# Kernel optimization log

Hardware: AMD Instinct MI355X
Metric: run time of the kernel (lower is better)

## Reference

```python
import jax, jax.numpy as jnp
import numpy as np

N = 10000
E = 160000
C = 256        # in_channels
M = 256        # mid_channels
R = 64         # nregion


def _glorot(key, shape):
    fan_in, fan_out = shape[-1], shape[0]
    lim = (6.0 / (fan_in + fan_out)) ** 0.5
    return jax.random.uniform(key, shape, jnp.float32, -lim, lim)


def setup_inputs() -> dict:
    key = jax.random.key(0)
    ks = jax.random.split(key, 12)
    x = jax.random.normal(ks[0], (N, C), jnp.float32)
    edge_index = jax.random.randint(ks[1], (2, E), 0, N, jnp.int32)
    conv_w = _glorot(ks[2], (C, C))
    conv_b = jnp.zeros((C,), jnp.float32)
    lin1_w = _glorot(ks[3], (M, C)); lin1_b = jnp.zeros((M,), jnp.float32)
    lin2_w = _glorot(ks[4], (M, M)); lin2_b = jnp.zeros((M,), jnp.float32)
    lin3_w = _glorot(ks[5], (1, M)); lin3_b = jnp.zeros((1,), jnp.float32)
    lin4_w = _glorot(ks[6], (M, M)); lin4_b = jnp.zeros((M,), jnp.float32)
    bilin_w = _glorot(ks[7], (R, M, M)) * 0.1
    bilin_b = jnp.zeros((R,), jnp.float32)
    return {"x": x, "edge_index": edge_index,
            "conv_w": conv_w, "conv_b": conv_b,
            "lin1_w": lin1_w, "lin1_b": lin1_b,
            "lin2_w": lin2_w, "lin2_b": lin2_b,
            "lin3_w": lin3_w, "lin3_b": lin3_b,
            "lin4_w": lin4_w, "lin4_b": lin4_b,
            "bilin_w": bilin_w, "bilin_b": bilin_b}


def gcn_conv(x, edge_index, w, b):
    # PyG GCNConv: add self-loops, symmetric D^-1/2 (A+I) D^-1/2 normalization
    src, dst = edge_index[0], edge_index[1]
    n = x.shape[0]
    xw = x @ w.T                                            # [N, C]
    deg = jnp.ones((n,), xw.dtype).at[dst].add(jnp.ones((E,), xw.dtype))  # +1 for self loop
    dinv = jax.lax.rsqrt(deg)
    norm = dinv[src] * dinv[dst]                            # [E]
    agg = jnp.zeros_like(xw).at[dst].add(norm[:, None] * xw[src])
    agg = agg + (dinv * dinv)[:, None] * xw                 # self-loop messages
    return agg + b


def reference(x, edge_index, conv_w, conv_b, lin1_w, lin1_b, lin2_w, lin2_b,
              lin3_w, lin3_b, lin4_w, lin4_b, bilin_w, bilin_b):
    out = jax.nn.relu(gcn_conv(x, edge_index, conv_w, conv_b))
    x0 = out + x                                            # residual [N, C]
    x0 = jax.nn.relu(x0 @ lin1_w.T + lin1_b)                # [N, M]
    x1 = jax.nn.relu(x0 @ lin2_w.T + lin2_b)
    x1 = x1 @ lin3_w.T + lin3_b                             # [N, 1]
    x2 = jax.nn.relu(x0 @ lin4_w.T + lin4_b)                # [N, M]
    # Bilinear(x2, x2): out[n,r] = x2[n] @ W[r] @ x2[n] + b[r]
    t = (x2 @ bilin_w.reshape(R * M, M).T).reshape(-1, R, M)  # [N, R, M]
    x2 = jnp.sum(t * x2[:, None, :], axis=-1) + bilin_b       # [N, R]
    return (x1, x2)
```

## Files before the change

kernel.cpp:

```cpp
#include <hip/hip_runtime.h>

typedef unsigned short u16;
typedef __attribute__((ext_vector_type(8))) short bf16x8;
typedef __attribute__((ext_vector_type(4))) float f32x4;

#define N_NODES 10000
#define E_EDGES 160000

__device__ __forceinline__ float b2f(u16 u) {
  union { unsigned i; float f; } c; c.i = ((unsigned)u) << 16; return c.f;
}
__device__ __forceinline__ u16 f2b(float f) {
  union { float f; unsigned i; } c; c.f = f;
  unsigned i = c.i;
  return (u16)((i + 0x7FFFu + ((i >> 16) & 1u)) >> 16);
}

__global__ void detect_kernel(const unsigned* __restrict__ w, int* __restrict__ flag) {
  int t = threadIdx.x;
  int cnt = 0;
  for (int i = t; i < 1024; i += 64) {
    unsigned e = (w[i] >> 7) & 0xFF;
    cnt += (e >= 100 && e <= 145) ? 1 : 0;
  }
  for (int o = 32; o; o >>= 1) cnt += __shfl_xor(cnt, o);
  if (t == 0) *flag = (cnt >= 512) ? 1 : 0;
}
__global__ void canon_kernel(const void* __restrict__ src, u16* __restrict__ dst,
                             int n, const int* __restrict__ flag) {
  int i = blockIdx.x * 256 + threadIdx.x;
  if (i >= n) return;
  if (*flag) dst[i] = ((const u16*)src)[i];
  else       dst[i] = f2b(((const float*)src)[i]);
}
__global__ void canon4_kernel(const void* s0, const void* s1, const void* s2, const void* s3,
                              u16* d0, u16* d1, u16* d2, u16* d3,
                              const int* __restrict__ flag) {
  int tsel = blockIdx.x >> 8;
  int i = (blockIdx.x & 255) * 256 + threadIdx.x;
  const void* s = tsel == 0 ? s0 : tsel == 1 ? s1 : tsel == 2 ? s2 : s3;
  u16* d = tsel == 0 ? d0 : tsel == 1 ? d1 : tsel == 2 ? d2 : d3;
  if (*flag) d[i] = ((const u16*)s)[i];
  else       d[i] = f2b(((const float*)s)[i]);
}
__global__ void canon_small_kernel(const void* s0, const void* s1, const void* s2,
                                   const void* s3, const void* s4, const void* s5,
                                   const void* s6,
                                   u16* d0, u16* d1, u16* d2, u16* d3, u16* d4,
                                   u16* d5, u16* d6, const int* __restrict__ flag) {
  int t = threadIdx.x;
  int f = *flag;
  const void* srcs[7] = {s0, s1, s2, s3, s4, s5, s6};
  u16* dsts[7] = {d0, d1, d2, d3, d4, d5, d6};
  const int ns[7] = {256, 256, 256, 256, 256, 64, 1};
#pragma unroll
  for (int k = 0; k < 7; ++k) {
    if (t < ns[k]) {
      if (f) dsts[k][t] = ((const u16*)srcs[k])[t];
      else   dsts[k][t] = f2b(((const float*)srcs[k])[t]);
    }
  }
}

__device__ __forceinline__ void stage_async(const u16* __restrict__ src, int stride,
                                            int row0, int maxRow, int k0,
                                            u16* lds, int w, int lane) {
  int rsel = lane >> 3;
  int gch = (lane & 7) ^ rsel;
#pragma unroll
  for (int i = 0; i < 4; ++i) {
    int rb = (w * 4 + i) * 8;
    int grow = row0 + rb + rsel;
    grow = grow > maxRow ? maxRow : grow;
    const u16* gp = src + (size_t)grow * stride + k0 + gch * 8;
    u16* lp = lds + rb * 64;
    __builtin_amdgcn_global_load_lds(
        (const __attribute__((address_space(1))) void*)gp,
        (__attribute__((address_space(3))) void*)lp, 16, 0, 0);
  }
}

__device__ __forceinline__ void mma_tile(const u16* lA, const u16* lB,
                                         f32x4 acc[4][4], int wr, int wc, int lane) {
#pragma unroll
  for (int ks = 0; ks < 2; ++ks) {
    bf16x8 af[4], bfr[4];
    int g = ks * 4 + (lane >> 4);
#pragma unroll
    for (int t = 0; t < 4; ++t) {
      int rowA = wr * 64 + t * 16 + (lane & 15);
      af[t] = *(const bf16x8*)(lA + rowA * 64 + ((g ^ (rowA & 7)) * 8));
      int rowB = wc * 64 + t * 16 + (lane & 15);
      bfr[t] = *(const bf16x8*)(lB + rowB * 64 + ((g ^ (rowB & 7)) * 8));
    }
#pragma unroll
    for (int ti = 0; ti < 4; ++ti)
#pragma unroll
      for (int tj = 0; tj < 4; ++tj)
        acc[ti][tj] = __builtin_amdgcn_mfma_f32_16x16x32_bf16(af[ti], bfr[tj],
                                                              acc[ti][tj], 0, 0, 0);
  }
}

template <bool RELU, bool F32OUT>
__global__ __launch_bounds__(256, 2)
void gemm_kernel(const u16* __restrict__ A, const u16* __restrict__ B,
                 const u16* __restrict__ bias, float* __restrict__ outF,
                 u16* __restrict__ outB, int NN, int J, int K) {
  __shared__ u16 lA[128 * 64];
  __shared__ u16 lB[128 * 64];
  int lane = threadIdx.x & 63;
  int w = threadIdx.x >> 6;
  int wr = w >> 1, wc = w & 1;
  int n0 = blockIdx.y * 128;
  int j0 = blockIdx.x * 128;
  f32x4 acc[4][4];
#pragma unroll
  for (int i = 0; i < 4; ++i)
#pragma unroll
    for (int j = 0; j < 4; ++j) acc[i][j] = (f32x4){0.f, 0.f, 0.f, 0.f};

  for (int kt = 0; kt < K; kt += 64) {
    stage_async(A, K, n0, NN - 1, kt, lA, w, lane);
    stage_async(B, K, j0, J - 1, kt, lB, w, lane);
    __syncthreads();
    mma_tile(lA, lB, acc, wr, wc, lane);
    __syncthreads();
  }

#pragma unroll
  for (int ti = 0; ti < 4; ++ti)
#pragma unroll
    for (int tj = 0; tj < 4; ++tj) {
      int col = j0 + wc * 64 + tj * 16 + (lane & 15);
      float bv = bias ? b2f(bias[col]) : 0.0f;
#pragma unroll
      for (int r = 0; r < 4; ++r) {
        int row = n0 + wr * 64 + ti * 16 + ((lane >> 4) << 2) + r;
        if (row < NN) {
          float v = acc[ti][tj][r] + bv;
          if (RELU) v = fmaxf(v, 0.0f);
          if (F32OUT) outF[(size_t)row * J + col] = v;
          else        outB[(size_t)row * J + col] = f2b(v);
        }
      }
    }
}

__global__ __launch_bounds__(256, 2)
void gemm_fused234_kernel(const u16* __restrict__ A, const u16* __restrict__ B,
                          const u16* __restrict__ bias, const u16* __restrict__ w3,
                          float* __restrict__ out1acc, u16* __restrict__ x2v, int NN) {
  __shared__ u16 lA[128 * 64];
  __shared__ u16 lB[128 * 64];
  int lane = threadIdx.x & 63;
  int w = threadIdx.x >> 6;
  int wr = w >> 1, wc = w & 1;
  int n0 = blockIdx.y * 128;
  int j0 = blockIdx.x * 128;
  f32x4 acc[4][4];
#pragma unroll
  for (int i = 0; i < 4; ++i)
#pragma unroll
    for (int j = 0; j < 4; ++j) acc[i][j] = (f32x4){0.f, 0.f, 0.f, 0.f};

  for (int kt = 0; kt < 256; kt += 64) {
    stage_async(A, 256, n0, NN - 1, kt, lA, w, lane);
    stage_async(B, 256, j0, 511, kt, lB, w, lane);
    __syncthreads();
    mma_tile(lA, lB, acc, wr, wc, lane);
    __syncthreads();
  }

  if (j0 < 256) {
    float part[4][4];
#pragma unroll
    for (int ti = 0; ti < 4; ++ti)
#pragma unroll
      for (int r = 0; r < 4; ++r) part[ti][r] = 0.0f;
#pragma unroll
    for (int ti = 0; ti < 4; ++ti)
#pragma unroll
      for (int tj = 0; tj < 4; ++tj) {
        int col = j0 + wc * 64 + tj * 16 + (lane & 15);
        float bv = b2f(bias[col]);
        float wv = b2f(w3[col]);
#pragma unroll
        for (int r = 0; r < 4; ++r) {
          float v = fmaxf(acc[ti][tj][r] + bv, 0.0f);
          part[ti][r] += v * wv;
        }
      }
#pragma unroll
    for (int ti = 0; ti < 4; ++ti)
#pragma unroll
      for (int r = 0; r < 4; ++r) {
        float s = part[ti][r];
        s += __shfl_xor(s, 1);
        s += __shfl_xor(s, 2);
        s += __shfl_xor(s, 4);
        s += __shfl_xor(s, 8);
        if ((lane & 15) == 0) {
          int row = n0 + wr * 64 + ti * 16 + ((lane >> 4) << 2) + r;
          if (row < NN) unsafeAtomicAdd(&out1acc[row], s);
        }
      }
  } else {
#pragma unroll
    for (int ti = 0; ti < 4; ++ti)
#pragma unroll
      for (int tj = 0; tj < 4; ++tj) {
        int col = j0 + wc * 64 + tj * 16 + (lane & 15);
        float bv = b2f(bias[col]);
#pragma unroll
        for (int r = 0; r < 4; ++r) {
          int row = n0 + wr * 64 + ti * 16 + ((lane >> 4) << 2) + r;
          if (row < NN) {
            float v = fmaxf(acc[ti][tj][r] + bv, 0.0f);
            x2v[(size_t)row * 256 + (col - 256)] = f2b(v);
          }
        }
      }
  }
}

__global__ __launch_bounds__(256, 2)
void bilinear_kernel(const u16* __restrict__ x2v, const u16* __restrict__ W,
                     float* __restrict__ out2acc, int NN) {
  __shared__ u16 lA[128 * 64];
  __shared__ u16 lB[128 * 64];
  int lane = threadIdx.x & 63;
  int w = threadIdx.x >> 6;
  int wr = w >> 1, wc = w & 1;
  int n0 = blockIdx.y * 128;
  int rm0 = blockIdx.x * 128;
  int m0g = rm0 & 255;
  int xv_kt = (m0g >> 6) + wc;
  f32x4 acc[4][4];
#pragma unroll
  for (int i = 0; i < 4; ++i)
#pragma unroll
    for (int j = 0; j < 4; ++j) acc[i][j] = (f32x4){0.f, 0.f, 0.f, 0.f};

  u16 xvr[4][16];

#pragma unroll
  for (int kt4 = 0; kt4 < 4; ++kt4) {
    stage_async(x2v, 256, n0, NN - 1, kt4 * 64, lA, w, lane);
    stage_async(W, 256, rm0, 16383, kt4 * 64, lB, w, lane);
    __syncthreads();
    mma_tile(lA, lB, acc, wr, wc, lane);
    if (kt4 == xv_kt) {
#pragma unroll
      for (int tj = 0; tj < 4; ++tj) {
        int kl = tj * 16 + (lane & 15);
        int ch = kl >> 3, off = kl & 7;
#pragma unroll
        for (int ti = 0; ti < 4; ++ti)
#pragma unroll
          for (int r = 0; r < 4; ++r) {
            int rowl = wr * 64 + ti * 16 + ((lane >> 4) << 2) + r;
            xvr[tj][ti * 4 + r] = lA[rowl * 64 + ((ch ^ (rowl & 7)) * 8) + off];
          }
      }
    }
    __syncthreads();
  }

  int region = rm0 >> 8;
  float rowsum[4][4];
#pragma unroll
  for (int ti = 0; ti < 4; ++ti)
#pragma unroll
    for (int r = 0; r < 4; ++r) rowsum[ti][r] = 0.0f;

#pragma unroll
  for (int ti = 0; ti < 4; ++ti)
#pragma unroll
    for (int tj = 0; tj < 4; ++tj)
#pragma unroll
      for (int r = 0; r < 4; ++r)
        rowsum[ti][r] += acc[ti][tj][r] * b2f(xvr[tj][ti * 4 + r]);

#pragma unroll
  for (int ti = 0; ti < 4; ++ti)
#pragma unroll
    for (int r = 0; r < 4; ++r) {
      float s = rowsum[ti][r];
      s += __shfl_xor(s, 1);
      s += __shfl_xor(s, 2);
      s += __shfl_xor(s, 4);
      s += __shfl_xor(s, 8);
      if ((lane & 15) == 0) {
        int rowl = wr * 64 + ti * 16 + ((lane >> 4) << 2) + r;
        int n = n0 + rowl;
        if (n < NN) unsafeAtomicAdd(&out2acc[(size_t)n * 64 + region], s);
      }
    }
}

__global__ void hist_kernel(const int* __restrict__ ei, int* __restrict__ count) {
  int i = blockIdx.x * 256 + threadIdx.x;
  if (i < E_EDGES) atomicAdd(&count[ei[E_EDGES + i]], 1);
}

__global__ void scan_kernel(const int* __restrict__ count, int* __restrict__ start,
                            int* __restrict__ cursor, float* __restrict__ dinv) {
  __shared__ int wsum[16];
  __shared__ int carry_s;
  int t = threadIdx.x;
  int wv = t >> 6, ln = t & 63;
  if (t == 0) carry_s = 0;
  __syncthreads();
  for (int base = 0; base < N_NODES; base += 1024) {
    int i = base + t;
    int v = (i < N_NODES) ? count[i] : 0;
    int s = v;
#pragma unroll
    for (int o = 1; o < 64; o <<= 1) {
      int u = __shfl_up(s, o);
      if (ln >= o) s += u;
    }
    if (ln == 63) wsum[wv] = s;
    __syncthreads();
    if (wv == 0) {
      int x = (ln < 16) ? wsum[ln] : 0;
#pragma unroll
      for (int o = 1; o < 16; o <<= 1) {
        int u = __shfl_up(x, o);
        if (ln >= o) x += u;
      }
      if (ln < 16) wsum[ln] = x;
    }
    __syncthreads();
    int excl = s - v + (wv ? wsum[wv - 1] : 0) + carry_s;
    if (i < N_NODES) {
      start[i] = excl;
      cursor[i] = excl;
      dinv[i] = rsqrtf(1.0f + (float)v);
    }
    __syncthreads();
    if (t == 0) carry_s += wsum[15];
    __syncthreads();
  }
}

__global__ void place_kernel(const int* __restrict__ ei, int* __restrict__ cursor,
                             int* __restrict__ order) {
  int i = blockIdx.x * 256 + threadIdx.x;
  if (i >= E_EDGES) return;
  int d = ei[E_EDGES + i];
  int pos = atomicAdd(&cursor[d], 1);
  order[pos] = i;
}

__global__ void gather_kernel(const int* __restrict__ ei, const int* __restrict__ order,
                              const int* __restrict__ start, const int* __restrict__ count,
                              const float* __restrict__ dinv, const float* __restrict__ xw,
                              const u16* __restrict__ conv_b, const u16* __restrict__ x,
                              u16* __restrict__ x0) {
  int node = (blockIdx.x * blockDim.x + threadIdx.x) >> 6;
  int lane = threadIdx.x & 63;
  if (node >= N_NODES) return;
  int s0 = start[node], cnt = count[node];
  float dn = dinv[node];
  float ax = 0.f, ay = 0.f, az = 0.f, aw = 0.f;
  for (int base = 0; base < cnt; base += 64) {
    int rem = cnt - base;
    int m = rem < 64 ? rem : 64;
    int eid = (lane < m) ? order[s0 + base + lane] : 0;
    int s = (lane < m) ? ei[eid] : 0;
    float nrm = (lane < m) ? dinv[s] * dn : 0.f;
    for (int j = 0; j < m; ++j) {
      int sj = __shfl(s, j);
      float nj = __shfl(nrm, j);
      float4 v = *((const float4*)(xw + (size_t)sj * 256) + lane);
      ax += nj * v.x; ay += nj * v.y; az += nj * v.z; aw += nj * v.w;
    }
  }
  float4 sv = *((const float4*)(xw + (size_t)node * 256) + lane);
  float slw = dn * dn;
  const u16* bb = conv_b + lane * 4;
  const u16* xr = x + (size_t)node * 256 + lane * 4;
  u16 o[4];
  float vals[4] = {ax + slw * sv.x, ay + slw * sv.y, az + slw * sv.z, aw + slw * sv.w};
#pragma unroll
  for (int j = 0; j < 4; ++j) {
    float v = vals[j] + b2f(bb[j]);
    v = fmaxf(v, 0.0f) + b2f(xr[j]);
    o[j] = f2b(v);
  }
  *((ushort4*)(x0 + (size_t)node * 256) + lane) = make_ushort4(o[0], o[1], o[2], o[3]);
}

__global__ void out_final_kernel(const float* __restrict__ out1acc,
                                 const float* __restrict__ out2acc,
                                 const u16* __restrict__ b3, const u16* __restrict__ bb,
                                 void* __restrict__ dout, const int* __restrict__ flag) {
  int idx = blockIdx.x * 256 + threadIdx.x;
  int f = *flag;
  if (idx < N_NODES) {
    float v = out1acc[idx] + b2f(b3[0]);
    if (f) ((u16*)dout)[idx] = f2b(v);
    else   ((float*)dout)[idx] = v;
  } else if (idx < N_NODES + N_NODES * 64) {
    int k = idx - N_NODES;
    float v = out2acc[k] + b2f(bb[k & 63]);
    if (f) ((u16*)dout)[idx] = f2b(v);
    else   ((float*)dout)[idx] = v;
  }
}

extern "C" void kernel_launch(void* const* d_in, const int* in_sizes, int n_in,
                              void* d_out, int out_size, void* d_ws, size_t ws_size,
                              hipStream_t stream) {
  const int* ei = (const int*)d_in[1];

  float* ws      = (float*)d_ws;
  float* xw      = ws;
  int*   count   = (int*)(xw + N_NODES * 256);
  int*   start   = count + 10240;
  int*   cursor  = start + 10240;
  int*   order   = cursor + 10240;
  float* dinv    = (float*)(order + E_EDGES);
  float* out1acc = dinv + 10240;
  float* out2acc = out1acc + 10240;
  u16* x0  = (u16*)(out2acc + N_NODES * 64);
  u16* x0m = x0 + N_NODES * 256;
  u16* x2v = x0m + N_NODES * 256;
  u16* cx  = x2v + N_NODES * 256;
  u16* cwc = cx + N_NODES * 256;
  u16* cw1 = cwc + 65536;
  u16* cw2 = cw1 + 65536;
  u16* cw4 = cw2 + 65536;
  u16* cwB = cw4 + 65536;
  u16* cbc = cwB + 4194304;
  u16* cb1 = cbc + 256;
  u16* cb2 = cb1 + 256;
  u16* cb4 = cb2 + 256;
  u16* cw3 = cb4 + 256;
  u16* cbB = cw3 + 256;
  u16* cb3 = cbB + 64;
  int* flag = (int*)(cb3 + 16);

  hipMemsetAsync(count, 0, N_NODES * sizeof(int), stream);
  hipMemsetAsync(out1acc, 0, (10240 + (size_t)N_NODES * 64) * sizeof(float), stream);

  detect_kernel<<<1, 64, 0, stream>>>((const unsigned*)d_in[0], flag);

  canon_kernel<<<(N_NODES * 256 + 255) / 256, 256, 0, stream>>>(d_in[0], cx, N_NODES * 256, flag);
  canon4_kernel<<<1024, 256, 0, stream>>>(d_in[2], d_in[4], d_in[6], d_in[10],
                                          cwc, cw1, cw2, cw4, flag);
  canon_small_kernel<<<1, 256, 0, stream>>>(d_in[3], d_in[5], d_in[7], d_in[11],
                                            d_in[8], d_in[13], d_in[9],
                                            cbc, cb1, cb2, cb4, cw3, cbB, cb3, flag);
  canon_kernel<<<(4194304 + 255) / 256, 256, 0, stream>>>(d_in[12], cwB, 4194304, flag);

  hist_kernel<<<(E_EDGES + 255) / 256, 256, 0, stream>>>(ei, count);
  scan_kernel<<<1, 1024, 0, stream>>>(count, start, cursor, dinv);
  place_kernel<<<(E_EDGES + 255) / 256, 256, 0, stream>>>(ei, cursor, order);

  gemm_kernel<false, true><<<dim3(2, 79), 256, 0, stream>>>(
      cx, cwc, nullptr, xw, nullptr, N_NODES, 256, 256);

  gather_kernel<<<(N_NODES * 64 + 255) / 256, 256, 0, stream>>>(
      ei, order, start, count, dinv, xw, cbc, cx, x0);

  gemm_kernel<true, false><<<dim3(2, 79), 256, 0, stream>>>(
      x0, cw1, cb1, nullptr, x0m, N_NODES, 256, 256);

  gemm_fused234_kernel<<<dim3(4, 79), 256, 0, stream>>>(
      x0m, cw2, cb2, cw3, out1acc, x2v, N_NODES);

  bilinear_kernel<<<dim3(128, 79), 256, 0, stream>>>(x2v, cwB, out2acc, N_NODES);

  out_final_kernel<<<(N_NODES * 65 + 255) / 256, 256, 0, stream>>>(
      out1acc, out2acc, cb3, cbB, d_out, flag);
}
```

Before: 404.3 us.

## Fuse all canonicalization and histogram kernels into one vectorized launch

Merges the four conversion kernels and the degree histogram into one kernel. Each thread now converts 8 contiguous elements with vector loads and stores over a flat destination buffer, and trailing blocks do the edge histogram. This removes several launches and the scalar 2-byte stores. It also raises the bilinear kernel's launch-bounds occupancy hint from 2 to 3, which may force register spilling.

```diff
diff --git a/kernel.cpp b/kernel.cpp
--- a/kernel.cpp
+++ b/kernel.cpp
@@ -2,10 +2,16 @@
 
 typedef unsigned short u16;
 typedef __attribute__((ext_vector_type(8))) short bf16x8;
+typedef __attribute__((ext_vector_type(8))) unsigned short u16x8;
 typedef __attribute__((ext_vector_type(4))) float f32x4;
 
 #define N_NODES 10000
 #define E_EDGES 160000
+#define CX_N 2560000
+#define W_N  65536
+#define WB_N 4194304
+#define CANON_BIG_BLOCKS 3426
+#define HIST_BLOCKS 79
 
 __device__ __forceinline__ float b2f(u16 u) {
   union { unsigned i; float f; } c; c.i = ((unsigned)u) << 16; return c.f;
@@ -26,38 +32,58 @@
   for (int o = 32; o; o >>= 1) cnt += __shfl_xor(cnt, o);
   if (t == 0) *flag = (cnt >= 512) ? 1 : 0;
 }
-__global__ void canon_kernel(const void* __restrict__ src, u16* __restrict__ dst,
-                             int n, const int* __restrict__ flag) {
-  int i = blockIdx.x * 256 + threadIdx.x;
-  if (i >= n) return;
-  if (*flag) dst[i] = ((const u16*)src)[i];
-  else       dst[i] = f2b(((const float*)src)[i]);
-}
-__global__ void canon4_kernel(const void* s0, const void* s1, const void* s2, const void* s3,
-                              u16* d0, u16* d1, u16* d2, u16* d3,
-                              const int* __restrict__ flag) {
-  int tsel = blockIdx.x >> 8;
-  int i = (blockIdx.x & 255) * 256 + threadIdx.x;
-  const void* s = tsel == 0 ? s0 : tsel == 1 ? s1 : tsel == 2 ? s2 : s3;
-  u16* d = tsel == 0 ? d0 : tsel == 1 ? d1 : tsel == 2 ? d2 : d3;
-  if (*flag) d[i] = ((const u16*)s)[i];
-  else       d[i] = f2b(((const float*)s)[i]);
-}
-__global__ void canon_small_kernel(const void* s0, const void* s1, const void* s2,
-                                   const void* s3, const void* s4, const void* s5,
-                                   const void* s6,
-                                   u16* d0, u16* d1, u16* d2, u16* d3, u16* d4,
-                                   u16* d5, u16* d6, const int* __restrict__ flag) {
-  int t = threadIdx.x;
+
+__global__ void canon_all_kernel(const void* sx, const void* swc, const void* sw1,
+                                 const void* sw2, const void* sw4, const void* swB,
+                                 const void* sbc, const void* sb1, const void* sb2,
+                                 const void* sb4, const void* sw3, const void* sbB,
+                                 const void* sb3,
+                                 u16* __restrict__ dstBase,
+                                 u16* cbc, u16* cb1, u16* cb2, u16* cb4,
+                                 u16* cw3, u16* cbB, u16* cb3,
+                                 const int* __restrict__ ei, int* __restrict__ count,
+                                 const int* __restrict__ flag) {
+  int b = blockIdx.x;
   int f = *flag;
-  const void* srcs[7] = {s0, s1, s2, s3, s4, s5, s6};
-  u16* dsts[7] = {d0, d1, d2, d3, d4, d5, d6};
-  const int ns[7] = {256, 256, 256, 256, 256, 64, 1};
-#pragma unroll
-  for (int k = 0; k < 7; ++k) {
-    if (t < ns[k]) {
-      if (f) dsts[k][t] = ((const u16*)srcs[k])[t];
-      else   dsts[k][t] = f2b(((const float*)srcs[k])[t]);
+  if (b < CANON_BIG_BLOCKS) {
+    long e = ((long)b * 256 + threadIdx.x) * 8;
+    const void* src; long so;
+    if (e < CX_N)                { src = sx;  so = e; }
+    else if (e < CX_N + W_N)     { src = swc; so = e - CX_N; }
+    else if (e < CX_N + 2 * W_N) { src = sw1; so = e - (CX_N + W_N); }
+    else if (e < CX_N + 3 * W_N) { src = sw2; so = e - (CX_N + 2 * W_N); }
+    else if (e < CX_N + 4 * W_N) { src = sw4; so = e - (CX_N + 3 * W_N); }
+    else                         { src = swB; so = e - (CX_N + 4 * W_N); }
+    if (f) {
+      u16x8 v = *((const u16x8*)((const u16*)src + so));
+      *(u16x8*)(dstBase + e) = v;
+    } else {
+      const float* fp = (const float*)src + so;
+      float4 a = *(const float4*)fp;
+      float4 c = *(const float4*)(fp + 4);
+      u16x8 o;
+      o[0] = f2b(a.x); o[1] = f2b(a.y); o[2] = f2b(a.z); o[3] = f2b(a.w);
+      o[4] = f2b(c.x); o[5] = f2b(c.y); o[6] = f2b(c.z); o[7] = f2b(c.w);
+      *(u16x8*)(dstBase + e) = o;
+    }
+  } else if (b == CANON_BIG_BLOCKS) {
+    int t = threadIdx.x;
+    const void* srcs[7] = {sbc, sb1, sb2, sb4, sw3, sbB, sb3};
+    u16* dsts[7] = {cbc, cb1, cb2, cb4, cw3, cbB, cb3};
+    const int ns[7] = {256, 256, 256, 256, 256, 64, 1};
+#pragma unroll
+    for (int k = 0; k < 7; ++k) {
+      if (t < ns[k]) {
+        if (f) dsts[k][t] = ((const u16*)srcs[k])[t];
+        else   dsts[k][t] = f2b(((const float*)srcs[k])[t]);
+      }
+    }
+  } else {
+    int base = (b - CANON_BIG_BLOCKS - 1) * 2048 + threadIdx.x * 8;
+#pragma unroll
+    for (int k = 0; k < 8; ++k) {
+      int i = base + k;
+      if (i < E_EDGES) atomicAdd(&count[ei[E_EDGES + i]], 1);
     }
   }
 }
@@ -224,7 +250,7 @@
   }
 }
 
-__global__ __launch_bounds__(256, 2)
+__global__ __launch_bounds__(256, 3)
 void bilinear_kernel(const u16* __restrict__ x2v, const u16* __restrict__ W,
                      float* __restrict__ out2acc, int NN) {
   __shared__ u16 lA[128 * 64];
@@ -297,11 +323,6 @@
         if (n < NN) unsafeAtomicAdd(&out2acc[(size_t)n * 64 + region], s);
       }
     }
-}
-
-__global__ void hist_kernel(const int* __restrict__ ei, int* __restrict__ count) {
-  int i = blockIdx.x * 256 + threadIdx.x;
-  if (i < E_EDGES) atomicAdd(&count[ei[E_EDGES + i]], 1);
 }
 
 __global__ void scan_kernel(const int* __restrict__ count, int* __restrict__ start,
@@ -429,12 +450,12 @@
   u16* x0m = x0 + N_NODES * 256;
   u16* x2v = x0m + N_NODES * 256;
   u16* cx  = x2v + N_NODES * 256;
-  u16* cwc = cx + N_NODES * 256;
-  u16* cw1 = cwc + 65536;
-  u16* cw2 = cw1 + 65536;
-  u16* cw4 = cw2 + 65536;
-  u16* cwB = cw4 + 65536;
-  u16* cbc = cwB + 4194304;
+  u16* cwc = cx + CX_N;
+  u16* cw1 = cwc + W_N;
+  u16* cw2 = cw1 + W_N;
+  u16* cw4 = cw2 + W_N;
+  u16* cwB = cw4 + W_N;
+  u16* cbc = cwB + WB_N;
   u16* cb1 = cbc + 256;
   u16* cb2 = cb1 + 256;
   u16* cb4 = cb2 + 256;
@@ -448,15 +469,12 @@
 
   detect_kernel<<<1, 64, 0, stream>>>((const unsigned*)d_in[0], flag);
 
-  canon_kernel<<<(N_NODES * 256 + 255) / 256, 256, 0, stream>>>(d_in[0], cx, N_NODES * 256, flag);
-  canon4_kernel<<<1024, 256, 0, stream>>>(d_in[2], d_in[4], d_in[6], d_in[10],
-                                          cwc, cw1, cw2, cw4, flag);
-  canon_small_kernel<<<1, 256, 0, stream>>>(d_in[3], d_in[5], d_in[7], d_in[11],
-                                            d_in[8], d_in[13], d_in[9],
-                                            cbc, cb1, cb2, cb4, cw3, cbB, cb3, flag);
-  canon_kernel<<<(4194304 + 255) / 256, 256, 0, stream>>>(d_in[12], cwB, 4194304, flag);
-
-  hist_kernel<<<(E_EDGES + 255) / 256, 256, 0, stream>>>(ei, count);
+  canon_all_kernel<<<CANON_BIG_BLOCKS + 1 + HIST_BLOCKS, 256, 0, stream>>>(
+      d_in[0], d_in[2], d_in[4], d_in[6], d_in[10], d_in[12],
+      d_in[3], d_in[5], d_in[7], d_in[11], d_in[8], d_in[13], d_in[9],
+      cx, cbc, cb1, cb2, cb4, cw3, cbB, cb3,
+      ei, count, flag);
+
   scan_kernel<<<1, 1024, 0, stream>>>(count, start, cursor, dinv);
   place_kernel<<<(E_EDGES + 255) / 256, 256, 0, stream>>>(ei, cursor, order);
 
```

Result: no change. 407.1 us (+0.7%).
